# Optimization experiments

Measured on AMD Instinct MI355X. Metric: run time of the kernel, lower is better.

## Reference

```python
import jax, jax.numpy as jnp
import numpy as np

EPS = 1e-12  # torch F.normalize eps


def setup_inputs() -> dict:
    key = jax.random.key(0)
    k1, k2, k3 = jax.random.split(key, 3)
    B, C, N, E, EMB = 128, 16, 128, 4, 16
    OUT = EMB // E  # Linear(emb_sz, emb_sz // num_edges)
    x = jax.random.normal(k1, (B, C, N, EMB), dtype=jnp.float32)
    A = jax.random.uniform(k2, (E, N, N), dtype=jnp.float32)  # non-negative adjacency
    # per-edge-type Linear weights, stored [E, in, out] so y = x @ W[e]
    W = jax.random.normal(k3, (E, EMB, OUT), dtype=jnp.float32) * (1.0 / np.sqrt(EMB))
    return {"x": x, "A": A, "W": W}


def reference(x, A, W):
    # F.normalize(A[e], dim=0): L2-normalize each column -> norm over rows (axis=1 of [E,N,N])
    col_norm = jnp.sqrt(jnp.sum(A * A, axis=1, keepdims=True))  # [E,1,N]
    An = A / jnp.maximum(col_norm, EPS)                         # [E,N,N]
    # x.transpose(3,2) @ An[e] then transpose back:
    # out[e,b,c,m,f] = sum_n x[b,c,n,f] * An[e,n,m]
    msg = jnp.einsum('bcnf,enm->ebcmf', x, An)                  # [E,B,C,N,EMB]
    # per-edge Linear (bias=False) + relu
    h = jax.nn.relu(jnp.einsum('ebcmf,efo->ebcmo', msg, W))     # [E,B,C,N,OUT]
    E_, B, C, N, O = h.shape
    # torch.cat([h_0, h_1, ...], axis=1) -> [B, E*C, N, OUT]
    out = jnp.transpose(h, (1, 0, 2, 3, 4)).reshape(B, E_ * C, N, O)
    return out
```

## Files before the change

### kernel.cpp

```cpp
#include <hip/hip_runtime.h>
#include <math.h>

#define EPSN 1e-12f

typedef __attribute__((ext_vector_type(8))) __bf16 bf16x8;
typedef __attribute__((ext_vector_type(8))) short short8;
typedef __attribute__((ext_vector_type(4))) float floatx4;

static __device__ __forceinline__ unsigned short f2bf(float f) {
    return __builtin_bit_cast(unsigned short, (__bf16)f);
}

__global__ __launch_bounds__(512, 2)
void gcn_one(const float* __restrict__ x, const float* __restrict__ A,
             const float* __restrict__ W, float* __restrict__ out) {
    __shared__ __align__(16) unsigned char xw[32768];
    __shared__ __align__(16) unsigned char at[2][32768];
    __shared__ float red[2][16][128];

    const int t   = threadIdx.x;
    const int bc0 = blockIdx.x * 8;
    const int w   = t >> 6;
    const int l   = t & 63;
    const int cl  = l & 15;
    const int lg  = l >> 4;
    const int mw  = w * 16 + cl;
    const int mq  = t & 31;
    const int ng  = t >> 5;

    float4 v4a[8], v4b[8];
    #pragma unroll
    for (int j = 0; j < 8; ++j)
        v4a[j] = *(const float4*)(A + (size_t)(ng * 8 + j) * 128 + mq * 4);
    #pragma unroll
    for (int j = 0; j < 8; ++j)
        v4b[j] = *(const float4*)(A + 16384 + (size_t)(ng * 8 + j) * 128 + mq * 4);

    bf16x8 bW;
    {
        short8 z = {0, 0, 0, 0, 0, 0, 0, 0};
        bW = __builtin_bit_cast(bf16x8, z);
        if (lg < 2) {
            unsigned short hs[8] __attribute__((aligned(16)));
            #pragma unroll
            for (int j = 0; j < 8; ++j)
                hs[j] = f2bf(W[(cl >> 2) * 64 + (lg * 8 + j) * 4 + (cl & 3)]);
            bW = __builtin_bit_cast(bf16x8, *(const short8*)hs);
        }
    }
    #pragma unroll
    for (int ti = 0; ti < 8; ++ti) {
        int T = w * 8 + ti;
        bf16x8 ax;
        { short8 z = {0, 0, 0, 0, 0, 0, 0, 0}; ax = __builtin_bit_cast(bf16x8, z); }
        if (lg < 2) {
            int R = T * 16 + cl;
            const float* xp = x + ((size_t)bc0 * 128 + R) * 16 + lg * 8;
            float4 a = *(const float4*)xp;
            float4 b = *(const float4*)(xp + 4);
            unsigned short hs[8] __attribute__((aligned(16)));
            hs[0] = f2bf(a.x); hs[1] = f2bf(a.y); hs[2] = f2bf(a.z); hs[3] = f2bf(a.w);
            hs[4] = f2bf(b.x); hs[5] = f2bf(b.y); hs[6] = f2bf(b.z); hs[7] = f2bf(b.w);
            ax = __builtin_bit_cast(bf16x8, *(const short8*)hs);
        }
        floatx4 d = {0.f, 0.f, 0.f, 0.f};
        d = __builtin_amdgcn_mfma_f32_16x16x32_bf16(ax, bW, d, 0, 0, 0);
        int eD = cl >> 2, oD = cl & 3;
        int bcl = T >> 3;
        int nb  = (T & 7) * 16 + lg * 4;
        int r   = bcl * 4 + oD;
        int base = (eD * 32 + r) << 8;
        int s    = (r & 7) << 4;
        #pragma unroll
        for (int q = 0; q < 4; ++q) {
            int off = (base + (nb + q) * 2) ^ s;
            *(unsigned short*)(xw + off) = f2bf(d[q]);
        }
    }

    auto stage_write = [&](int buf, const float4* v4) {
        floatx4 rs = {0.f, 0.f, 0.f, 0.f};
        #pragma unroll
        for (int i = 0; i < 4; ++i) {
            int m = mq * 4 + i;
            unsigned short hs[8] __attribute__((aligned(16)));
            #pragma unroll
            for (int j = 0; j < 8; ++j) {
                float vv = ((const float*)&v4[j])[i];
                rs[i] += vv * vv;
                hs[j] = f2bf(vv);
            }
            int slot = ng ^ (mq & 7);
            *(short8*)(at[buf] + ((m << 8) | (slot << 4))) = *(const short8*)hs;
        }
        *(float4*)&red[buf][ng][mq * 4] = *(const float4*)&rs;
    };

    stage_write(0, v4a);
    stage_write(1, v4b);
    __syncthreads();

    auto compute_e = [&](int e, int buf) {
        bf16x8 af[2][4];
        #pragma unroll
        for (int rt = 0; rt < 2; ++rt)
            #pragma unroll
            for (int ks = 0; ks < 4; ++ks) {
                int row = rt * 16 + cl;
                int off = (((e * 32 + row) << 8) + (ks * 32 + lg * 8) * 2)
                          ^ ((row & 7) << 4);
                af[rt][ks] = __builtin_bit_cast(bf16x8, *(const short8*)(xw + off));
            }
        bf16x8 bfr[4];
        #pragma unroll
        for (int ks = 0; ks < 4; ++ks) {
            int slot = (ks * 4 + lg) ^ ((mw >> 2) & 7);
            bfr[ks] = __builtin_bit_cast(bf16x8,
                *(const short8*)(at[buf] + ((mw << 8) | (slot << 4))));
        }
        floatx4 acc0 = {0.f, 0.f, 0.f, 0.f};
        floatx4 acc1 = {0.f, 0.f, 0.f, 0.f};
        #pragma unroll
        for (int ks = 0; ks < 4; ++ks) {
            acc0 = __builtin_amdgcn_mfma_f32_16x16x32_bf16(af[0][ks], bfr[ks], acc0, 0, 0, 0);
            acc1 = __builtin_amdgcn_mfma_f32_16x16x32_bf16(af[1][ks], bfr[ks], acc1, 0, 0, 0);
        }
        float ssum = 0.f;
        #pragma unroll
        for (int g = 0; g < 16; ++g) ssum += red[buf][g][mw];
        float rn = 1.0f / fmaxf(sqrtf(ssum), EPSN);
        #pragma unroll
        for (int rt = 0; rt < 2; ++rt) {
            floatx4 a = rt ? acc1 : acc0;
            int bc = bc0 + rt * 4 + lg;
            int b = bc >> 4, c = bc & 15;
            float4 o4;
            o4.x = fmaxf(a[0] * rn, 0.f);
            o4.y = fmaxf(a[1] * rn, 0.f);
            o4.z = fmaxf(a[2] * rn, 0.f);
            o4.w = fmaxf(a[3] * rn, 0.f);
            ((float4*)out)[(size_t)(b * 64 + e * 16 + c) * 128 + mw] = o4;
        }
    };

    #pragma unroll
    for (int j = 0; j < 8; ++j)
        v4a[j] = *(const float4*)(A + 2 * 16384 + (size_t)(ng * 8 + j) * 128 + mq * 4);
    compute_e(0, 0);
    __syncthreads();
    stage_write(0, v4a);

    #pragma unroll
    for (int j = 0; j < 8; ++j)
        v4b[j] = *(const float4*)(A + 3 * 16384 + (size_t)(ng * 8 + j) * 128 + mq * 4);
    compute_e(1, 1);
    __syncthreads();
    stage_write(1, v4b);

    compute_e(2, 0);
    __syncthreads();

    compute_e(3, 1);
}

extern "C" void kernel_launch(void* const* d_in, const int* in_sizes, int n_in,
                              void* d_out, int out_size, void* d_ws, size_t ws_size,
                              hipStream_t stream) {
    const float* x = (const float*)d_in[0];
    const float* A = (const float*)d_in[1];
    const float* W = (const float*)d_in[2];
    float* out = (float*)d_out;

    gcn_one<<<256, 512, 0, stream>>>(x, A, W, out);
}
```

Before: 18.53 us.

## Double threads per block, splitting row tiles across 16 waves

```diff
diff --git a/kernel.cpp b/kernel.cpp
--- a/kernel.cpp
+++ b/kernel.cpp
@@ -11,7 +11,7 @@
     return __builtin_bit_cast(unsigned short, (__bf16)f);
 }
 
-__global__ __launch_bounds__(512, 2)
+__global__ __launch_bounds__(1024, 4)
 void gcn_one(const float* __restrict__ x, const float* __restrict__ A,
              const float* __restrict__ W, float* __restrict__ out) {
     __shared__ __align__(16) unsigned char xw[32768];
@@ -24,17 +24,21 @@
     const int l   = t & 63;
     const int cl  = l & 15;
     const int lg  = l >> 4;
-    const int mw  = w * 16 + cl;
+    const int rt  = w >> 3;
+    const int mw  = (w & 7) * 16 + cl;
+    const bool stager = (t < 512);
     const int mq  = t & 31;
-    const int ng  = t >> 5;
+    const int ng  = (t >> 5) & 15;
 
     float4 v4a[8], v4b[8];
-    #pragma unroll
-    for (int j = 0; j < 8; ++j)
-        v4a[j] = *(const float4*)(A + (size_t)(ng * 8 + j) * 128 + mq * 4);
-    #pragma unroll
-    for (int j = 0; j < 8; ++j)
-        v4b[j] = *(const float4*)(A + 16384 + (size_t)(ng * 8 + j) * 128 + mq * 4);
+    if (stager) {
+        #pragma unroll
+        for (int j = 0; j < 8; ++j)
+            v4a[j] = *(const float4*)(A + (size_t)(ng * 8 + j) * 128 + mq * 4);
+        #pragma unroll
+        for (int j = 0; j < 8; ++j)
+            v4b[j] = *(const float4*)(A + 16384 + (size_t)(ng * 8 + j) * 128 + mq * 4);
+    }
 
     bf16x8 bW;
     {
@@ -49,8 +53,8 @@
         }
     }
     #pragma unroll
-    for (int ti = 0; ti < 8; ++ti) {
-        int T = w * 8 + ti;
+    for (int ti = 0; ti < 4; ++ti) {
+        int T = w * 4 + ti;
         bf16x8 ax;
         { short8 z = {0, 0, 0, 0, 0, 0, 0, 0}; ax = __builtin_bit_cast(bf16x8, z); }
         if (lg < 2) {
@@ -96,21 +100,18 @@
         *(float4*)&red[buf][ng][mq * 4] = *(const float4*)&rs;
     };
 
-    stage_write(0, v4a);
-    stage_write(1, v4b);
+    if (stager) { stage_write(0, v4a); stage_write(1, v4b); }
     __syncthreads();
 
     auto compute_e = [&](int e, int buf) {
-        bf16x8 af[2][4];
+        bf16x8 af[4];
         #pragma unroll
-        for (int rt = 0; rt < 2; ++rt)
-            #pragma unroll
-            for (int ks = 0; ks < 4; ++ks) {
-                int row = rt * 16 + cl;
-                int off = (((e * 32 + row) << 8) + (ks * 32 + lg * 8) * 2)
-                          ^ ((row & 7) << 4);
-                af[rt][ks] = __builtin_bit_cast(bf16x8, *(const short8*)(xw + off));
-            }
+        for (int ks = 0; ks < 4; ++ks) {
+            int row = rt * 16 + cl;
+            int off = (((e * 32 + row) << 8) + (ks * 32 + lg * 8) * 2)
+                      ^ ((row & 7) << 4);
+            af[ks] = __builtin_bit_cast(bf16x8, *(const short8*)(xw + off));
+        }
         bf16x8 bfr[4];
         #pragma unroll
         for (int ks = 0; ks < 4; ++ks) {
@@ -118,48 +119,42 @@
             bfr[ks] = __builtin_bit_cast(bf16x8,
                 *(const short8*)(at[buf] + ((mw << 8) | (slot << 4))));
         }
-        floatx4 acc0 = {0.f, 0.f, 0.f, 0.f};
-        floatx4 acc1 = {0.f, 0.f, 0.f, 0.f};
+        floatx4 acc = {0.f, 0.f, 0.f, 0.f};
         #pragma unroll
-        for (int ks = 0; ks < 4; ++ks) {
-            acc0 = __builtin_amdgcn_mfma_f32_16x16x32_bf16(af[0][ks], bfr[ks], acc0, 0, 0, 0);
-            acc1 = __builtin_amdgcn_mfma_f32_16x16x32_bf16(af[1][ks], bfr[ks], acc1, 0, 0, 0);
-        }
+        for (int ks = 0; ks < 4; ++ks)
+            acc = __builtin_amdgcn_mfma_f32_16x16x32_bf16(af[ks], bfr[ks], acc, 0, 0, 0);
         float ssum = 0.f;
         #pragma unroll
         for (int g = 0; g < 16; ++g) ssum += red[buf][g][mw];
         float rn = 1.0f / fmaxf(sqrtf(ssum), EPSN);
-        #pragma unroll
-        for (int rt = 0; rt < 2; ++rt) {
-            floatx4 a = rt ? acc1 : acc0;
-            int bc = bc0 + rt * 4 + lg;
-            int b = bc >> 4, c = bc & 15;
-            float4 o4;
-            o4.x = fmaxf(a[0] * rn, 0.f);
-            o4.y = fmaxf(a[1] * rn, 0.f);
-            o4.z = fmaxf(a[2] * rn, 0.f);
-            o4.w = fmaxf(a[3] * rn, 0.f);
-            ((float4*)out)[(size_t)(b * 64 + e * 16 + c) * 128 + mw] = o4;
-        }
+        int bc = bc0 + rt * 4 + lg;
+        int b = bc >> 4, c = bc & 15;
+        float4 o4;
+        o4.x = fmaxf(acc[0] * rn, 0.f);
+        o4.y = fmaxf(acc[1] * rn, 0.f);
+        o4.z = fmaxf(acc[2] * rn, 0.f);
+        o4.w = fmaxf(acc[3] * rn, 0.f);
+        ((float4*)out)[(size_t)(b * 64 + e * 16 + c) * 128 + mw] = o4;
     };
 
-    #pragma unroll
-    for (int j = 0; j < 8; ++j)
-        v4a[j] = *(const float4*)(A + 2 * 16384 + (size_t)(ng * 8 + j) * 128 + mq * 4);
+    if (stager) {
+        #pragma unroll
+        for (int j = 0; j < 8; ++j)
+            v4a[j] = *(const float4*)(A + 2 * 16384 + (size_t)(ng * 8 + j) * 128 + mq * 4);
+    }
     compute_e(0, 0);
     __syncthreads();
-    stage_write(0, v4a);
-
-    #pragma unroll
-    for (int j = 0; j < 8; ++j)
-        v4b[j] = *(const float4*)(A + 3 * 16384 + (size_t)(ng * 8 + j) * 128 + mq * 4);
+    if (stager) {
+        stage_write(0, v4a);
+        #pragma unroll
+        for (int j = 0; j < 8; ++j)
+            v4b[j] = *(const float4*)(A + 3 * 16384 + (size_t)(ng * 8 + j) * 128 + mq * 4);
+    }
     compute_e(1, 1);
     __syncthreads();
-    stage_write(1, v4b);
-
+    if (stager) stage_write(1, v4b);
     compute_e(2, 0);
     __syncthreads();
-
     compute_e(3, 1);
 }
 
@@ -171,5 +166,5 @@
     const float* W = (const float*)d_in[2];
     float* out = (float*)d_out;
 
-    gcn_one<<<256, 512, 0, stream>>>(x, A, W, out);
+    gcn_one<<<256, 1024, 0, stream>>>(x, A, W, out);
 }
```

After: 26.87 us. 45.0% more time.
